# Optimization experiments

Hardware: AMD Instinct MI355X
Metric: run time of the kernel (lower is better)

Reference implementation:

```python
import jax, jax.numpy as jnp
import numpy as np

V = 196608          # 12 * nside^2, nside = 128 (HEALPix)
DEG = 9             # ~8 neighbors + diagonal
NNZ = V * DEG
K = 3               # Chebyshev order (kernel_size)
C_IN, C_MID, C_OUT = 16, 32, 32
B = 2
EPS = 1e-5


def _spmv(rows, cols, vals, x):
    """Sparse Laplacian mat-vec over the vertex dim. x: [B, V, F]."""
    Bn, Vn, F = x.shape
    y = x.transpose(1, 0, 2).reshape(Vn, Bn * F)          # [V, B*F]
    gathered = y[cols] * vals[:, None]                    # [NNZ, B*F] irregular gather
    out = jax.ops.segment_sum(gathered, rows, num_segments=Vn)
    return out.reshape(Vn, Bn, F).transpose(1, 0, 2)      # [B, V, F]


def _cheb_conv(rows, cols, vals, x, W):
    """K-order Chebyshev conv. W: [K, Fin, Fout]."""
    x0 = x
    x1 = _spmv(rows, cols, vals, x0)
    xs = [x0, x1]
    for _ in range(W.shape[0] - 2):
        xs.append(2.0 * _spmv(rows, cols, vals, xs[-1]) - xs[-2])
    stack = jnp.stack(xs)                                  # [K, B, V, Fin]
    return jnp.einsum('kbvf,kfo->bvo', stack, W)


def _bn_relu(x, gamma, beta):
    """BatchNorm over (batch, vertices) per channel (training stats), then ReLU."""
    mean = x.mean(axis=(0, 1))
    var = x.var(axis=(0, 1))  # biased, as torch BN uses for normalization
    return jax.nn.relu((x - mean) * jax.lax.rsqrt(var + EPS) * gamma + beta)


def setup_inputs() -> dict:
    key = jax.random.key(0)
    ks = jax.random.split(key, 8)
    x = jax.random.normal(ks[0], (B, V, C_IN), dtype=jnp.float32)
    rows = jnp.repeat(jnp.arange(V, dtype=jnp.int64), DEG)              # sorted row indices
    cols = jax.random.randint(ks[1], (NNZ,), 0, V).astype(jnp.int64)
    vals = jax.random.normal(ks[2], (NNZ,), dtype=jnp.float32) * 0.1
    W1 = jax.random.normal(ks[3], (K, C_IN, C_MID), dtype=jnp.float32) * 0.05
    W2 = jax.random.normal(ks[4], (K, C_MID, C_OUT), dtype=jnp.float32) * 0.05
    g1 = jnp.ones((C_MID,), dtype=jnp.float32)
    b1 = jnp.zeros((C_MID,), dtype=jnp.float32)
    g2 = jnp.ones((C_OUT,), dtype=jnp.float32)
    b2 = jnp.zeros((C_OUT,), dtype=jnp.float32)
    return {"x": x, "rows": rows, "cols": cols, "vals": vals,
            "W1": W1, "g1": g1, "b1": b1, "W2": W2, "g2": g2, "b2": b2}


def reference(x, rows, cols, vals, W1, g1, b1, W2, g2, b2):
    h = _cheb_conv(rows, cols, vals, x, W1)
    h = _bn_relu(h, g1, b1)
    h = _cheb_conv(rows, cols, vals, h, W2)
    h = _bn_relu(h, g2, b2)
    return h
```

## Files before the change

### kernel.cpp

```cpp
#include <hip/hip_runtime.h>
#include <hip/hip_bf16.h>

#define Vn 196608
#define DEG 9
#define BV 393216
#define NNZ 1769472
constexpr float EPS = 1e-5f;

typedef unsigned short u16;
using short8 = __attribute__((ext_vector_type(8))) short;
using f32x4  = __attribute__((ext_vector_type(4))) float;

__device__ __forceinline__ float b2f(u16 h) { return __uint_as_float((unsigned)h << 16); }
__device__ __forceinline__ u16 f2b(float f) {
    unsigned u = __float_as_uint(f);
    return (u16)((u + 0x7FFFu + ((u >> 16) & 1u)) >> 16);
}

template<int FF> __device__ __forceinline__ float ldfT(const void* p, int i, int rt) {
    if constexpr (FF == 1) return ((const float*)p)[i];
    else if constexpr (FF == 0) return b2f(((const u16*)p)[i]);
    else return rt ? ((const float*)p)[i] : b2f(((const u16*)p)[i]);
}
template<int FI> __device__ __forceinline__ int ldcT(const void* p, int i, int rt) {
    if constexpr (FI == 1) return (int)((const long long*)p)[i];
    else if constexpr (FI == 0) return ((const int*)p)[i];
    else return rt ? (int)((const long long*)p)[i] : ((const int*)p)[i];
}

__global__ void k0_probe(const void* g1, const void* cols, int* flags, float* zf) {
    int tid = threadIdx.x;
    if (tid < 256) zf[tid] = 0.f;
    if (tid == 0) {
        const unsigned short* gw = (const unsigned short*)g1;
        int zc = 0;
        for (int i = 0; i < 32; i += 2) if (gw[i] == 0) ++zc;
        flags[0] = (zc >= 8) ? 1 : 0;
        const unsigned int* cw = (const unsigned int*)cols;
        int zodd = 0;
        for (int i = 1; i < 64; i += 2) if (cw[i] == 0) ++zodd;
        flags[1] = (zodd >= 16) ? 1 : 0;
    }
}

template<int FF, int FI>
__global__ void __launch_bounds__(256) k1_spmv1(const void* __restrict__ x,
                                                const void* __restrict__ cols,
                                                const void* __restrict__ vals,
                                                const int* __restrict__ flags,
                                                u16* __restrict__ y1) {
    int t = blockIdx.x * 256 + threadIdx.x;
    int rF = 0, rI = 0;
    if constexpr (FF == 2) { rF = flags[0]; rI = flags[1]; }
    int v = t >> 5;
    int b = (t >> 4) & 1;
    int f = t & 15;
    int e0 = v * DEG;
    int xb = b * (Vn * 16);
    float acc = 0.f;
#pragma unroll
    for (int e = 0; e < DEG; ++e) {
        int   c = ldcT<FI>(cols, e0 + e, rI);
        float w = ldfT<FF>(vals, e0 + e, rF);
        acc += w * ldfT<FF>(x, xb + c * 16 + f, rF);
    }
    y1[t] = f2b(acc);
}

template<int FF, int FI>
__global__ void __launch_bounds__(256) k2_conv1(const void* __restrict__ x,
                                                const void* __restrict__ cols,
                                                const void* __restrict__ vals,
                                                const u16* __restrict__ y1,
                                                const void* __restrict__ W1,
                                                const int* __restrict__ flags,
                                                u16* __restrict__ h1,
                                                float* __restrict__ stats) {
    __shared__ float W1s[1536];
    __shared__ float shx[8][2][16], shy[8][2][16], shz[8][2][16];
    __shared__ float red[256];
    const int tid = threadIdx.x;
    int rF = 0, rI = 0;
    if constexpr (FF == 2) { rF = flags[0]; rI = flags[1]; }
    for (int i = tid; i < 1536; i += 256) W1s[i] = ldfT<FF>(W1, i, rF);
    __syncthreads();
    const int g = tid >> 5, lane = tid & 31;
    const int b = lane >> 4, f = lane & 15;
    float s_acc = 0.f, ss_acc = 0.f;
    const int stride = gridDim.x * 8;
    for (int v = blockIdx.x * 8 + g; v < Vn; v += stride) {
        int e0 = v * DEG;
        float acc = 0.f;
#pragma unroll
        for (int e = 0; e < DEG; ++e) {
            int   c = ldcT<FI>(cols, e0 + e, rI);
            float w = ldfT<FF>(vals, e0 + e, rF);
            acc += w * b2f(y1[c * 32 + lane]);
        }
        float x0 = ldfT<FF>(x, (b * Vn + v) * 16 + f, rF);
        shx[g][b][f] = x0;
        shy[g][b][f] = b2f(y1[v * 32 + lane]);
        shz[g][b][f] = 2.f * acc - x0;
        const int o = lane;
        float a0 = 0.f, a1 = 0.f;
#pragma unroll
        for (int f2 = 0; f2 < 16; ++f2) {
            float w0 = W1s[f2 * 32 + o];
            float w1 = W1s[512 + f2 * 32 + o];
            float w2 = W1s[1024 + f2 * 32 + o];
            a0 += shx[g][0][f2] * w0 + shy[g][0][f2] * w1 + shz[g][0][f2] * w2;
            a1 += shx[g][1][f2] * w0 + shy[g][1][f2] * w1 + shz[g][1][f2] * w2;
        }
        h1[v * 64 + o]      = f2b(a0);
        h1[v * 64 + 32 + o] = f2b(a1);
        s_acc  += a0 + a1;
        ss_acc += a0 * a0 + a1 * a1;
    }
    __syncthreads();
    red[tid] = s_acc;  __syncthreads();
    if (tid < 32) { float s = 0.f; for (int j = 0; j < 8; ++j) s += red[tid + 32 * j]; atomicAdd(&stats[tid], s); }
    __syncthreads();
    red[tid] = ss_acc; __syncthreads();
    if (tid < 32) { float s = 0.f; for (int j = 0; j < 8; ++j) s += red[tid + 32 * j]; atomicAdd(&stats[32 + tid], s); }
}

__global__ void k_finalize(const float* __restrict__ stats,
                           const void* __restrict__ gamma,
                           const void* __restrict__ beta,
                           const int* __restrict__ flags,
                           float* __restrict__ scsh) {
    int o = threadIdx.x;
    if (o < 32) {
        const int fF = flags[0];
        const float n = (float)BV;
        float mean = stats[o] / n;
        float var  = stats[32 + o] / n - mean * mean;
        var = fmaxf(var, 0.f);
        float rs = rsqrtf(var + EPS);
        float sc = ldfT<2>(gamma, o, fF) * rs;
        scsh[o]      = sc;
        scsh[32 + o] = ldfT<2>(beta, o, fF) - mean * sc;
    }
}

template<int FF, int FI>
__global__ void __launch_bounds__(256) k3_spmv2(const u16* __restrict__ h1,
                                                const void* __restrict__ cols,
                                                const void* __restrict__ vals,
                                                const int* __restrict__ flags,
                                                const float* __restrict__ scsh,
                                                u16* __restrict__ z1) {
    int t = blockIdx.x * 256 + threadIdx.x;
    int rF = 0, rI = 0;
    if constexpr (FF == 2) { rF = flags[0]; rI = flags[1]; }
    int v = t >> 6;
    int lane = t & 63;
    int f = lane & 31;
    float sc = scsh[f], sh = scsh[32 + f];
    int e0 = v * DEG;
    float acc = 0.f;
#pragma unroll
    for (int e = 0; e < DEG; ++e) {
        int   c = ldcT<FI>(cols, e0 + e, rI);
        float w = ldfT<FF>(vals, e0 + e, rF);
        float hv = b2f(h1[c * 64 + lane]);
        acc += w * fmaxf(0.f, hv * sc + sh);
    }
    z1[t] = f2b(acc);
}

template<int FF, int FI>
__global__ void __launch_bounds__(256) k4a_spmv3(const u16* __restrict__ h1,
                                                 const u16* __restrict__ z1,
                                                 const void* __restrict__ cols,
                                                 const void* __restrict__ vals,
                                                 const int* __restrict__ flags,
                                                 const float* __restrict__ scsh,
                                                 u16* __restrict__ hn_out,
                                                 u16* __restrict__ z2) {
    int t = blockIdx.x * 256 + threadIdx.x;
    int rF = 0, rI = 0;
    if constexpr (FF == 2) { rF = flags[0]; rI = flags[1]; }
    int v = t >> 6;
    int lane = t & 63;
    int f = lane & 31;
    float sc = scsh[f], sh = scsh[32 + f];
    int e0 = v * DEG;
    float acc = 0.f;
#pragma unroll
    for (int e = 0; e < DEG; ++e) {
        int   c = ldcT<FI>(cols, e0 + e, rI);
        float w = ldfT<FF>(vals, e0 + e, rF);
        acc += w * b2f(z1[c * 64 + lane]);
    }
    float hn = fmaxf(0.f, b2f(h1[v * 64 + lane]) * sc + sh);
    hn_out[t] = f2b(hn);
    z2[t] = f2b(2.f * acc - hn);
}

template<int FF>
__global__ void __launch_bounds__(256) k4b_mfma(const u16* __restrict__ hn,
                                                const u16* __restrict__ z1,
                                                const u16* __restrict__ z2,
                                                const void* __restrict__ W2,
                                                const int* __restrict__ flags,
                                                void* __restrict__ out, int outF,
                                                float* __restrict__ stats) {
    __shared__ float red[4][32];
    const int tid = threadIdx.x;
    int rF = 0;
    if constexpr (FF == 2) { rF = flags[0]; }
    const int lane = tid & 63;
    const int n = lane & 15, q = lane >> 4;
    const int wv = tid >> 6;
    short8 bf[3][2];
#pragma unroll
    for (int kc = 0; kc < 3; ++kc)
#pragma unroll
        for (int nt = 0; nt < 2; ++nt)
#pragma unroll
            for (int j = 0; j < 8; ++j)
                bf[kc][nt][j] = (short)f2b(ldfT<FF>(W2, (kc * 32 + q * 8 + j) * 32 + nt * 16 + n, rF));

    float s0 = 0.f, ss0 = 0.f, s1 = 0.f, ss1 = 0.f;
    const int ntile_cnt = BV / 16;
    const int wstride = gridDim.x * 4;
    for (int tile = blockIdx.x * 4 + wv; tile < ntile_cnt; tile += wstride) {
        const int p0 = tile * 16;
        const int arow = (p0 + n) * 32 + q * 8;
        short8 a0 = *(const short8*)&hn[arow];
        short8 a1 = *(const short8*)&z1[arow];
        short8 a2 = *(const short8*)&z2[arow];
        f32x4 c0 = {0.f, 0.f, 0.f, 0.f}, c1 = {0.f, 0.f, 0.f, 0.f};
        c0 = __builtin_amdgcn_mfma_f32_16x16x32_bf16(a0, bf[0][0], c0, 0, 0, 0);
        c0 = __builtin_amdgcn_mfma_f32_16x16x32_bf16(a1, bf[1][0], c0, 0, 0, 0);
        c0 = __builtin_amdgcn_mfma_f32_16x16x32_bf16(a2, bf[2][0], c0, 0, 0, 0);
        c1 = __builtin_amdgcn_mfma_f32_16x16x32_bf16(a0, bf[0][1], c1, 0, 0, 0);
        c1 = __builtin_amdgcn_mfma_f32_16x16x32_bf16(a1, bf[1][1], c1, 0, 0, 0);
        c1 = __builtin_amdgcn_mfma_f32_16x16x32_bf16(a2, bf[2][1], c1, 0, 0, 0);
#pragma unroll
        for (int r = 0; r < 4; ++r) {
            int p = p0 + q * 4 + r;
            int v = p >> 1, b = p & 1;
            int base = (b * Vn + v) * 32;
            float e0 = c0[r], e1 = c1[r];
            if (outF) { ((float*)out)[base + n] = e0; ((float*)out)[base + 16 + n] = e1; }
            else      { ((u16*)out)[base + n] = f2b(e0); ((u16*)out)[base + 16 + n] = f2b(e1); }
            s0 += e0; ss0 += e0 * e0;
            s1 += e1; ss1 += e1 * e1;
        }
    }
    s0  += __shfl_xor(s0, 16);  s0  += __shfl_xor(s0, 32);
    ss0 += __shfl_xor(ss0, 16); ss0 += __shfl_xor(ss0, 32);
    s1  += __shfl_xor(s1, 16);  s1  += __shfl_xor(s1, 32);
    ss1 += __shfl_xor(ss1, 16); ss1 += __shfl_xor(ss1, 32);
    if (q == 0) { red[wv][n] = s0; red[wv][16 + n] = s1; }
    __syncthreads();
    if (tid < 32) {
        float s = red[0][tid] + red[1][tid] + red[2][tid] + red[3][tid];
        atomicAdd(&stats[tid], s);
    }
    __syncthreads();
    if (q == 0) { red[wv][n] = ss0; red[wv][16 + n] = ss1; }
    __syncthreads();
    if (tid < 32) {
        float s = red[0][tid] + red[1][tid] + red[2][tid] + red[3][tid];
        atomicAdd(&stats[32 + tid], s);
    }
}

__global__ void __launch_bounds__(256) k5_norm(void* __restrict__ io, int outF,
                                               const float* __restrict__ scsh) {
    int t = blockIdx.x * 256 + threadIdx.x;
    if (outF) {
        float4* p = (float4*)io;
        float4 vv = p[t];
        int o = (t * 4) & 31;
        vv.x = fmaxf(0.f, vv.x * scsh[o]     + scsh[32 + o]);
        vv.y = fmaxf(0.f, vv.y * scsh[o + 1] + scsh[33 + o]);
        vv.z = fmaxf(0.f, vv.z * scsh[o + 2] + scsh[34 + o]);
        vv.w = fmaxf(0.f, vv.w * scsh[o + 3] + scsh[35 + o]);
        p[t] = vv;
    } else {
        u16* p = (u16*)io;
#pragma unroll
        for (int j = 0; j < 4; ++j) {
            int i = t * 4 + j;
            int o = i & 31;
            p[i] = f2b(fmaxf(0.f, b2f(p[i]) * scsh[o] + scsh[32 + o]));
        }
    }
}

static inline int alloc_size_class(const void* p, size_t small, size_t big) {
    hipDeviceptr_t base = nullptr; size_t sz = 0;
    if (hipMemGetAddressRange(&base, &sz, (hipDeviceptr_t)p) != hipSuccess || sz == 0) return -1;
    if (sz >= small && sz < small + 65536) return 0;
    if (sz >= big   && sz < big   + 65536) return 1;
    return -1;
}

extern "C" void kernel_launch(void* const* d_in, const int* in_sizes, int n_in,
                              void* d_out, int out_size, void* d_ws, size_t ws_size,
                              hipStream_t stream) {
    const void* x    = d_in[0];
    const void* cols = d_in[2];
    const void* vals = d_in[3];
    const void* W1   = d_in[4];
    const void* g1   = d_in[5];
    const void* b1   = d_in[6];
    const void* W2   = d_in[7];
    const void* g2   = d_in[8];
    const void* b2   = d_in[9];

    int outF = 1;
    {
        hipDeviceptr_t base = nullptr; size_t sz = 0;
        if (hipMemGetAddressRange(&base, &sz, (hipDeviceptr_t)d_out) == hipSuccess && sz != 0) {
            outF = (sz >= (size_t)out_size * 3) ? 1 : 0;
        }
    }
    int fI = alloc_size_class(cols, (size_t)NNZ * 4, (size_t)NNZ * 8);
    int fF = alloc_size_class(vals, (size_t)NNZ * 2, (size_t)NNZ * 4);

    char* ws = (char*)d_ws;
    int*   flags  = (int*)ws;
    float* zf     = (float*)(ws + 256);
    float* stats1 = zf;
    float* scsh1  = zf + 64;
    float* stats2 = zf + 128;
    float* scsh2  = zf + 192;
    size_t off = 2048;
    u16* y1 = (u16*)(ws + off); off += (size_t)Vn * 32 * 2;
    u16* h1 = (u16*)(ws + off); off += (size_t)Vn * 64 * 2;
    u16* z1 = (u16*)(ws + off); off += (size_t)Vn * 64 * 2;
    u16* z2 = (u16*)(ws + off); off += (size_t)Vn * 64 * 2;
    u16* hn = (u16*)(ws + off);

    k0_probe<<<1, 256, 0, stream>>>(g1, cols, flags, zf);

#define LAUNCH_ALL(FFv, FIv)                                                                  \
    do {                                                                                      \
        k1_spmv1<FFv, FIv><<<Vn * 32 / 256, 256, 0, stream>>>(x, cols, vals, flags, y1);      \
        k2_conv1<FFv, FIv><<<1536, 256, 0, stream>>>(x, cols, vals, y1, W1, flags, h1, stats1); \
        k_finalize<<<1, 64, 0, stream>>>(stats1, g1, b1, flags, scsh1);                       \
        k3_spmv2<FFv, FIv><<<Vn * 64 / 256, 256, 0, stream>>>(h1, cols, vals, flags, scsh1, z1); \
        k4a_spmv3<FFv, FIv><<<Vn * 64 / 256, 256, 0, stream>>>(h1, z1, cols, vals, flags, scsh1, hn, z2); \
        k4b_mfma<FFv><<<2048, 256, 0, stream>>>(hn, z1, z2, W2, flags, d_out, outF, stats2);  \
        k_finalize<<<1, 64, 0, stream>>>(stats2, g2, b2, flags, scsh2);                       \
        k5_norm<<<BV * 8 / 256, 256, 0, stream>>>(d_out, outF, scsh2);                        \
    } while (0)

    if      (fF == 0 && fI == 0) LAUNCH_ALL(0, 0);
    else if (fF == 0 && fI == 1) LAUNCH_ALL(0, 1);
    else if (fF == 1 && fI == 0) LAUNCH_ALL(1, 0);
    else if (fF == 1 && fI == 1) LAUNCH_ALL(1, 1);
    else                         LAUNCH_ALL(2, 2);
#undef LAUNCH_ALL
}
```

Before: 390.7 us.

## Split first Chebyshev conv into SpMV and MFMA kernels, pack input to bf16

The fused first-layer kernel, which did both the gather and a scalar LDS-based weight contraction, is split in two. One kernel does the second SpMV and writes y2; the other does the 3-term contraction with bf16 MFMA instructions and accumulates the BN statistics. A new pack kernel converts x into an interleaved bf16 [V,2,16] layout, so gathers read one contiguous 64-byte row per vertex instead of two strided fp32 rows. Separately, the second layer no longer materialises the normalized h buffer and recomputes BN+ReLU inside the MFMA kernel. This costs two extra launches and extra intermediate traffic, plus bf16 rounding of x.

```diff
diff --git a/kernel.cpp b/kernel.cpp
--- a/kernel.cpp
+++ b/kernel.cpp
@@ -43,8 +43,21 @@
     }
 }
 
+template<int FF>
+__global__ void __launch_bounds__(256) kxi_pack(const void* __restrict__ x,
+                                                const int* __restrict__ flags,
+                                                u16* __restrict__ xi) {
+    int t = blockIdx.x * 256 + threadIdx.x;
+    int rF = 0;
+    if constexpr (FF == 2) rF = flags[0];
+    int v = t >> 5;
+    int lane = t & 31;
+    int b = lane >> 4, f = lane & 15;
+    xi[t] = f2b(ldfT<FF>(x, (b * Vn + v) * 16 + f, rF));
+}
+
 template<int FF, int FI>
-__global__ void __launch_bounds__(256) k1_spmv1(const void* __restrict__ x,
+__global__ void __launch_bounds__(256) k1_spmv1(const u16* __restrict__ xi,
                                                 const void* __restrict__ cols,
                                                 const void* __restrict__ vals,
                                                 const int* __restrict__ flags,
@@ -53,75 +66,101 @@
     int rF = 0, rI = 0;
     if constexpr (FF == 2) { rF = flags[0]; rI = flags[1]; }
     int v = t >> 5;
-    int b = (t >> 4) & 1;
-    int f = t & 15;
+    int lane = t & 31;
     int e0 = v * DEG;
-    int xb = b * (Vn * 16);
     float acc = 0.f;
 #pragma unroll
     for (int e = 0; e < DEG; ++e) {
         int   c = ldcT<FI>(cols, e0 + e, rI);
         float w = ldfT<FF>(vals, e0 + e, rF);
-        acc += w * ldfT<FF>(x, xb + c * 16 + f, rF);
+        acc += w * b2f(xi[c * 32 + lane]);
     }
     y1[t] = f2b(acc);
 }
 
 template<int FF, int FI>
-__global__ void __launch_bounds__(256) k2_conv1(const void* __restrict__ x,
+__global__ void __launch_bounds__(256) k2a_spmv(const u16* __restrict__ xi,
+                                                const u16* __restrict__ y1,
                                                 const void* __restrict__ cols,
                                                 const void* __restrict__ vals,
+                                                const int* __restrict__ flags,
+                                                u16* __restrict__ y2) {
+    int t = blockIdx.x * 256 + threadIdx.x;
+    int rF = 0, rI = 0;
+    if constexpr (FF == 2) { rF = flags[0]; rI = flags[1]; }
+    int v = t >> 5;
+    int lane = t & 31;
+    int e0 = v * DEG;
+    float acc = 0.f;
+#pragma unroll
+    for (int e = 0; e < DEG; ++e) {
+        int   c = ldcT<FI>(cols, e0 + e, rI);
+        float w = ldfT<FF>(vals, e0 + e, rF);
+        acc += w * b2f(y1[c * 32 + lane]);
+    }
+    y2[t] = f2b(2.f * acc - b2f(xi[t]));
+}
+
+template<int FF>
+__global__ void __launch_bounds__(256) k2b_mfma(const u16* __restrict__ xi,
                                                 const u16* __restrict__ y1,
+                                                const u16* __restrict__ y2,
                                                 const void* __restrict__ W1,
                                                 const int* __restrict__ flags,
                                                 u16* __restrict__ h1,
                                                 float* __restrict__ stats) {
-    __shared__ float W1s[1536];
-    __shared__ float shx[8][2][16], shy[8][2][16], shz[8][2][16];
-    __shared__ float red[256];
+    __shared__ float red[4][32];
     const int tid = threadIdx.x;
-    int rF = 0, rI = 0;
-    if constexpr (FF == 2) { rF = flags[0]; rI = flags[1]; }
-    for (int i = tid; i < 1536; i += 256) W1s[i] = ldfT<FF>(W1, i, rF);
-    __syncthreads();
-    const int g = tid >> 5, lane = tid & 31;
-    const int b = lane >> 4, f = lane & 15;
-    float s_acc = 0.f, ss_acc = 0.f;
-    const int stride = gridDim.x * 8;
-    for (int v = blockIdx.x * 8 + g; v < Vn; v += stride) {
-        int e0 = v * DEG;
-        float acc = 0.f;
-#pragma unroll
-        for (int e = 0; e < DEG; ++e) {
-            int   c = ldcT<FI>(cols, e0 + e, rI);
-            float w = ldfT<FF>(vals, e0 + e, rF);
-            acc += w * b2f(y1[c * 32 + lane]);
+    int rF = 0;
+    if constexpr (FF == 2) rF = flags[0];
+    const int lane = tid & 63;
+    const int n = lane & 15, q = lane >> 4;
+    const int wv = tid >> 6;
+    short8 b1f[2], b2f_[2];
+#pragma unroll
+    for (int nt = 0; nt < 2; ++nt)
+#pragma unroll
+        for (int j = 0; j < 8; ++j) {
+            int k = q * 8 + j;
+            b1f[nt][j]  = (short)f2b(ldfT<FF>(W1, k * 32 + nt * 16 + n, rF));
+            b2f_[nt][j] = (k < 16) ? (short)f2b(ldfT<FF>(W1, (32 + k) * 32 + nt * 16 + n, rF)) : (short)0;
         }
-        float x0 = ldfT<FF>(x, (b * Vn + v) * 16 + f, rF);
-        shx[g][b][f] = x0;
-        shy[g][b][f] = b2f(y1[v * 32 + lane]);
-        shz[g][b][f] = 2.f * acc - x0;
-        const int o = lane;
-        float a0 = 0.f, a1 = 0.f;
-#pragma unroll
-        for (int f2 = 0; f2 < 16; ++f2) {
-            float w0 = W1s[f2 * 32 + o];
-            float w1 = W1s[512 + f2 * 32 + o];
-            float w2 = W1s[1024 + f2 * 32 + o];
-            a0 += shx[g][0][f2] * w0 + shy[g][0][f2] * w1 + shz[g][0][f2] * w2;
-            a1 += shx[g][1][f2] * w0 + shy[g][1][f2] * w1 + shz[g][1][f2] * w2;
+    const u16* a1base = (q < 2) ? xi : y1;
+    const int koff = (q & 1) * 8;
+    float s0 = 0.f, ss0 = 0.f, s1 = 0.f, ss1 = 0.f;
+    const int ntile_cnt = BV / 16;
+    const int wstride = gridDim.x * 4;
+    for (int tile = blockIdx.x * 4 + wv; tile < ntile_cnt; tile += wstride) {
+        const int p0 = tile * 16;
+        const int ar = (p0 + n) * 16 + koff;
+        short8 af1 = *(const short8*)&a1base[ar];
+        short8 af2 = *(const short8*)&y2[ar];
+        f32x4 c0 = {0.f, 0.f, 0.f, 0.f}, c1 = {0.f, 0.f, 0.f, 0.f};
+        c0 = __builtin_amdgcn_mfma_f32_16x16x32_bf16(af1, b1f[0],  c0, 0, 0, 0);
+        c0 = __builtin_amdgcn_mfma_f32_16x16x32_bf16(af2, b2f_[0], c0, 0, 0, 0);
+        c1 = __builtin_amdgcn_mfma_f32_16x16x32_bf16(af1, b1f[1],  c1, 0, 0, 0);
+        c1 = __builtin_amdgcn_mfma_f32_16x16x32_bf16(af2, b2f_[1], c1, 0, 0, 0);
+#pragma unroll
+        for (int r = 0; r < 4; ++r) {
+            int p = p0 + q * 4 + r;
+            float e0 = c0[r], e1 = c1[r];
+            h1[p * 32 + n]      = f2b(e0);
+            h1[p * 32 + 16 + n] = f2b(e1);
+            s0 += e0; ss0 += e0 * e0;
+            s1 += e1; ss1 += e1 * e1;
         }
-        h1[v * 64 + o]      = f2b(a0);
-        h1[v * 64 + 32 + o] = f2b(a1);
-        s_acc  += a0 + a1;
-        ss_acc += a0 * a0 + a1 * a1;
-    }
-    __syncthreads();
-    red[tid] = s_acc;  __syncthreads();
-    if (tid < 32) { float s = 0.f; for (int j = 0; j < 8; ++j) s += red[tid + 32 * j]; atomicAdd(&stats[tid], s); }
-    __syncthreads();
-    red[tid] = ss_acc; __syncthreads();
-    if (tid < 32) { float s = 0.f; for (int j = 0; j < 8; ++j) s += red[tid + 32 * j]; atomicAdd(&stats[32 + tid], s); }
+    }
+    s0  += __shfl_xor(s0, 16);  s0  += __shfl_xor(s0, 32);
+    ss0 += __shfl_xor(ss0, 16); ss0 += __shfl_xor(ss0, 32);
+    s1  += __shfl_xor(s1, 16);  s1  += __shfl_xor(s1, 32);
+    ss1 += __shfl_xor(ss1, 16); ss1 += __shfl_xor(ss1, 32);
+    if (q == 0) { red[wv][n] = s0; red[wv][16 + n] = s1; }
+    __syncthreads();
+    if (tid < 32) atomicAdd(&stats[tid], red[0][tid] + red[1][tid] + red[2][tid] + red[3][tid]);
+    __syncthreads();
+    if (q == 0) { red[wv][n] = ss0; red[wv][16 + n] = ss1; }
+    __syncthreads();
+    if (tid < 32) atomicAdd(&stats[32 + tid], red[0][tid] + red[1][tid] + red[2][tid] + red[3][tid]);
 }
 
 __global__ void k_finalize(const float* __restrict__ stats,
@@ -176,7 +215,6 @@
                                                  const void* __restrict__ vals,
                                                  const int* __restrict__ flags,
                                                  const float* __restrict__ scsh,
-                                                 u16* __restrict__ hn_out,
                                                  u16* __restrict__ z2) {
     int t = blockIdx.x * 256 + threadIdx.x;
     int rF = 0, rI = 0;
@@ -194,22 +232,22 @@
         acc += w * b2f(z1[c * 64 + lane]);
     }
     float hn = fmaxf(0.f, b2f(h1[v * 64 + lane]) * sc + sh);
-    hn_out[t] = f2b(hn);
     z2[t] = f2b(2.f * acc - hn);
 }
 
 template<int FF>
-__global__ void __launch_bounds__(256) k4b_mfma(const u16* __restrict__ hn,
+__global__ void __launch_bounds__(256) k4b_mfma(const u16* __restrict__ h1,
                                                 const u16* __restrict__ z1,
                                                 const u16* __restrict__ z2,
                                                 const void* __restrict__ W2,
                                                 const int* __restrict__ flags,
+                                                const float* __restrict__ scsh,
                                                 void* __restrict__ out, int outF,
                                                 float* __restrict__ stats) {
     __shared__ float red[4][32];
     const int tid = threadIdx.x;
     int rF = 0;
-    if constexpr (FF == 2) { rF = flags[0]; }
+    if constexpr (FF == 2) rF = flags[0];
     const int lane = tid & 63;
     const int n = lane & 15, q = lane >> 4;
     const int wv = tid >> 6;
@@ -221,6 +259,9 @@
 #pragma unroll
             for (int j = 0; j < 8; ++j)
                 bf[kc][nt][j] = (short)f2b(ldfT<FF>(W2, (kc * 32 + q * 8 + j) * 32 + nt * 16 + n, rF));
+    float scv[8], shv[8];
+#pragma unroll
+    for (int j = 0; j < 8; ++j) { scv[j] = scsh[q * 8 + j]; shv[j] = scsh[32 + q * 8 + j]; }
 
     float s0 = 0.f, ss0 = 0.f, s1 = 0.f, ss1 = 0.f;
     const int ntile_cnt = BV / 16;
@@ -228,7 +269,11 @@
     for (int tile = blockIdx.x * 4 + wv; tile < ntile_cnt; tile += wstride) {
         const int p0 = tile * 16;
         const int arow = (p0 + n) * 32 + q * 8;
-        short8 a0 = *(const short8*)&hn[arow];
+        short8 hv = *(const short8*)&h1[arow];
+        short8 a0;
+#pragma unroll
+        for (int j = 0; j < 8; ++j)
+            a0[j] = (short)f2b(fmaxf(0.f, b2f((u16)hv[j]) * scv[j] + shv[j]));
         short8 a1 = *(const short8*)&z1[arow];
         short8 a2 = *(const short8*)&z2[arow];
         f32x4 c0 = {0.f, 0.f, 0.f, 0.f}, c1 = {0.f, 0.f, 0.f, 0.f};
@@ -256,17 +301,11 @@
     ss1 += __shfl_xor(ss1, 16); ss1 += __shfl_xor(ss1, 32);
     if (q == 0) { red[wv][n] = s0; red[wv][16 + n] = s1; }
     __syncthreads();
-    if (tid < 32) {
-        float s = red[0][tid] + red[1][tid] + red[2][tid] + red[3][tid];
-        atomicAdd(&stats[tid], s);
-    }
+    if (tid < 32) atomicAdd(&stats[tid], red[0][tid] + red[1][tid] + red[2][tid] + red[3][tid]);
     __syncthreads();
     if (q == 0) { red[wv][n] = ss0; red[wv][16 + n] = ss1; }
     __syncthreads();
-    if (tid < 32) {
-        float s = red[0][tid] + red[1][tid] + red[2][tid] + red[3][tid];
-        atomicAdd(&stats[32 + tid], s);
-    }
+    if (tid < 32) atomicAdd(&stats[32 + tid], red[0][tid] + red[1][tid] + red[2][tid] + red[3][tid]);
 }
 
 __global__ void __launch_bounds__(256) k5_norm(void* __restrict__ io, int outF,
@@ -331,22 +370,25 @@
     float* stats2 = zf + 128;
     float* scsh2  = zf + 192;
     size_t off = 2048;
+    u16* xi = (u16*)(ws + off); off += (size_t)Vn * 32 * 2;
     u16* y1 = (u16*)(ws + off); off += (size_t)Vn * 32 * 2;
+    u16* y2 = (u16*)(ws + off); off += (size_t)Vn * 32 * 2;
     u16* h1 = (u16*)(ws + off); off += (size_t)Vn * 64 * 2;
     u16* z1 = (u16*)(ws + off); off += (size_t)Vn * 64 * 2;
-    u16* z2 = (u16*)(ws + off); off += (size_t)Vn * 64 * 2;
-    u16* hn = (u16*)(ws + off);
+    u16* z2 = (u16*)(ws + off);
 
     k0_probe<<<1, 256, 0, stream>>>(g1, cols, flags, zf);
 
 #define LAUNCH_ALL(FFv, FIv)                                                                  \
     do {                                                                                      \
-        k1_spmv1<FFv, FIv><<<Vn * 32 / 256, 256, 0, stream>>>(x, cols, vals, flags, y1);      \
-        k2_conv1<FFv, FIv><<<1536, 256, 0, stream>>>(x, cols, vals, y1, W1, flags, h1, stats1); \
+        kxi_pack<FFv><<<Vn * 32 / 256, 256, 0, stream>>>(x, flags, xi);                       \
+        k1_spmv1<FFv, FIv><<<Vn * 32 / 256, 256, 0, stream>>>(xi, cols, vals, flags, y1);     \
+        k2a_spmv<FFv, FIv><<<Vn * 32 / 256, 256, 0, stream>>>(xi, y1, cols, vals, flags, y2); \
+        k2b_mfma<FFv><<<2048, 256, 0, stream>>>(xi, y1, y2, W1, flags, h1, stats1);           \
         k_finalize<<<1, 64, 0, stream>>>(stats1, g1, b1, flags, scsh1);                       \
         k3_spmv2<FFv, FIv><<<Vn * 64 / 256, 256, 0, stream>>>(h1, cols, vals, flags, scsh1, z1); \
-        k4a_spmv3<FFv, FIv><<<Vn * 64 / 256, 256, 0, stream>>>(h1, z1, cols, vals, flags, scsh1, hn, z2); \
-        k4b_mfma<FFv><<<2048, 256, 0, stream>>>(hn, z1, z2, W2, flags, d_out, outF, stats2);  \
+        k4a_spmv3<FFv, FIv><<<Vn * 64 / 256, 256, 0, stream>>>(h1, z1, cols, vals, flags, scsh1, z2); \
+        k4b_mfma<FFv><<<2048, 256, 0, stream>>>(h1, z1, z2, W2, flags, scsh1, d_out, outF, stats2); \
         k_finalize<<<1, 64, 0, stream>>>(stats2, g2, b2, flags, scsh2);                       \
         k5_norm<<<BV * 8 / 256, 256, 0, stream>>>(d_out, outF, scsh2);                        \
     } while (0)
```

New measurement: 392.4 us. No clear change (+0.4%).
